# Kernel tuning notes

Hardware: AMD Instinct MI355X
Metric: run time of the kernel (lower is better)

Reference implementation:

```python
import jax, jax.numpy as jnp
import numpy as np

B, H, W, C = 2, 64, 128, 256
HEADS, K, HIDDEN = 8, 9, 1024
HD = C // HEADS
EPS = 1e-5


def _ln(z, g, b):
    m = z.mean(-1, keepdims=True)
    v = ((z - m) ** 2).mean(-1, keepdims=True)
    return (z - m) / jnp.sqrt(v + EPS) * g + b


def _bilinear(img, coords):
    # img: [hd, H, W]; coords: [H, W, K, 2] in [-1, 1] (x=width, y=height), align_corners=True
    Hh, Ww = img.shape[1], img.shape[2]
    cx = (coords[..., 0] + 1.0) * 0.5 * (Ww - 1)
    cy = (coords[..., 1] + 1.0) * 0.5 * (Hh - 1)
    x0 = jnp.floor(cx); y0 = jnp.floor(cy)
    wx = cx - x0; wy = cy - y0
    x0i = jnp.clip(x0, 0, Ww - 1).astype(jnp.int32)
    x1i = jnp.clip(x0 + 1, 0, Ww - 1).astype(jnp.int32)
    y0i = jnp.clip(y0, 0, Hh - 1).astype(jnp.int32)
    y1i = jnp.clip(y0 + 1, 0, Hh - 1).astype(jnp.int32)
    g = lambda yi, xi: img[:, yi, xi]  # [hd, H, W, K]
    return (g(y0i, x0i) * (1 - wy) * (1 - wx) + g(y0i, x1i) * (1 - wy) * wx
            + g(y1i, x0i) * wy * (1 - wx) + g(y1i, x1i) * wy * wx)


def setup_inputs() -> dict:
    key = jax.random.key(0)
    ks = jax.random.split(key, 12)
    s = 0.02
    return {
        "x": jax.random.normal(ks[0], (B, H * W, C), jnp.float32),
        "ref_point": jax.random.uniform(ks[1], (1, H, W, K, 2), jnp.float32, -1.0, 1.0),
        "ln1_g": jnp.ones((C,), jnp.float32), "ln1_b": jnp.zeros((C,), jnp.float32),
        "w_v": jax.random.normal(ks[2], (C, C), jnp.float32) * s, "b_v": jnp.zeros((C,), jnp.float32),
        "w_off": jax.random.normal(ks[3], (C, HEADS * K * 2), jnp.float32) * s, "b_off": jnp.zeros((HEADS * K * 2,), jnp.float32),
        "w_attn": jax.random.normal(ks[4], (C, HEADS * K), jnp.float32) * s, "b_attn": jnp.zeros((HEADS * K,), jnp.float32),
        "w_out": jax.random.normal(ks[5], (C, C), jnp.float32) * s, "b_out": jnp.zeros((C,), jnp.float32),
        "ln2_g": jnp.ones((C,), jnp.float32), "ln2_b": jnp.zeros((C,), jnp.float32),
        "w1": jax.random.normal(ks[6], (C, HIDDEN), jnp.float32) * s, "b1": jnp.zeros((HIDDEN,), jnp.float32),
        "w_dw": jax.random.normal(ks[7], (HIDDEN, 1, 3, 3), jnp.float32) * s, "b_dw": jnp.zeros((HIDDEN,), jnp.float32),
        "w2": jax.random.normal(ks[8], (HIDDEN, C), jnp.float32) * s, "b2": jnp.zeros((C,), jnp.float32),
    }


def reference(x, ref_point, ln1_g, ln1_b, w_v, b_v, w_off, b_off, w_attn, b_attn,
              w_out, b_out, ln2_g, ln2_b, w1, b1, w_dw, b_dw, w2, b2):
    # --- Sphere deformable self-attention branch ---
    xn = _ln(x, ln1_g, ln1_b).reshape(B, H, W, C)
    v = (xn @ w_v + b_v).reshape(B, H, W, HEADS, HD)
    v = jnp.transpose(v, (0, 3, 4, 1, 2))                               # [B, heads, hd, H, W]
    off = (xn @ w_off + b_off).reshape(B, H, W, HEADS, K, 2)
    locs = ref_point[:, :, :, None, :, :] + off                          # [B, H, W, heads, K, 2]
    locs = jnp.transpose(locs, (0, 3, 1, 2, 4, 5))                       # [B, heads, H, W, K, 2]
    attn = jax.nn.softmax((xn @ w_attn + b_attn).reshape(B, H, W, HEADS, K), axis=-1)
    sampled = jax.vmap(jax.vmap(_bilinear))(v, locs)                     # [B, heads, hd, H, W, K]
    agg = jnp.einsum('bndhwk,bhwnk->bhwnd', sampled, attn).reshape(B, H, W, C)
    x = x + ((agg @ w_out) + b_out).reshape(B, H * W, C)
    # --- LeFF branch: linear -> GELU -> circular-pad depthwise conv -> GELU -> linear ---
    y = _ln(x, ln2_g, ln2_b)
    h = jax.nn.gelu(y @ w1 + b1, approximate=False).reshape(B, H, W, HIDDEN)
    h = jnp.transpose(h, (0, 3, 1, 2))                                   # NCHW
    h = jnp.pad(h, ((0, 0), (0, 0), (0, 0), (1, 1)), mode='wrap')        # circular pad along width
    h = jnp.pad(h, ((0, 0), (0, 0), (1, 1), (0, 0)))                     # zero pad along height
    h = jax.lax.conv_general_dilated(h, w_dw, (1, 1), 'VALID',
                                     feature_group_count=HIDDEN,
                                     dimension_numbers=('NCHW', 'OIHW', 'NCHW'))
    h = jax.nn.gelu(h + b_dw[None, :, None, None], approximate=False)
    h = jnp.transpose(h, (0, 2, 3, 1)).reshape(B, H * W, HIDDEN)
    return x + h @ w2 + b2
```

## Files before the change

### kernel.cpp

```cpp
#include <hip/hip_runtime.h>
#include <hip/hip_bf16.h>
#include <hip/hip_fp8.h>
#include <type_traits>

constexpr int Bc = 2, Hc = 64, Wc = 128, Cc = 256;
constexpr int HEADS = 8, KPT = 9, HIDDEN = 1024;
constexpr int HD = Cc / HEADS;
constexpr int NPIX = Hc * Wc;
constexpr int Mrows = Bc * NPIX;
constexpr int NQKV = 512;

typedef __attribute__((ext_vector_type(4))) float f32x4;
typedef __attribute__((ext_vector_type(8))) short bf16x8;

__device__ __forceinline__ float bf2f(unsigned short u) {
    union { unsigned int i; float f; } c; c.i = ((unsigned int)u) << 16; return c.f;
}
__device__ __forceinline__ unsigned short f2bf(float f) {
    __hip_bfloat16 h = __float2bfloat16(f);
    return *reinterpret_cast<unsigned short*>(&h);
}
__device__ __forceinline__ unsigned char f2fp8(float f) {
    return __hip_fp8_e4m3(f).__x;
}
__device__ __forceinline__ float fp82f(unsigned char u) {
    __hip_fp8_e4m3 v; v.__x = u; return (float)v;
}
__device__ __forceinline__ float gelu_exact(float x) {
    return 0.5f * x * (1.0f + erff(x * 0.70710678118654752f));
}
__device__ __forceinline__ void gl2lds16(const void* g, void* l) {
    __builtin_amdgcn_global_load_lds(
        (const __attribute__((address_space(1))) unsigned int*)g,
        (__attribute__((address_space(3))) unsigned int*)l, 16, 0, 0);
}

__global__ __launch_bounds__(256) void prepln_kernel(
        const float* __restrict__ x, const float* __restrict__ ln1_g,
        const float* __restrict__ ln1_b, unsigned short* __restrict__ xn,
        const float* __restrict__ w_v, const float* __restrict__ b_v,
        const float* __restrict__ w_off, const float* __restrict__ b_off,
        const float* __restrict__ w_attn, const float* __restrict__ b_attn,
        const float* __restrict__ w_out, const float* __restrict__ w1,
        const float* __restrict__ w2, const float* __restrict__ w_dw,
        unsigned short* __restrict__ qkvT, float* __restrict__ qkvB,
        unsigned short* __restrict__ woutT, unsigned short* __restrict__ w1T,
        unsigned char* __restrict__ w2T8, float* __restrict__ wdwT) {
    const int t = threadIdx.x;
    if (blockIdx.x < Mrows / 4) {
        const int r = blockIdx.x * 4 + (t >> 6);
        const int l = t & 63;
        const size_t base = (size_t)r * Cc + l * 4;
        const float4 v = *reinterpret_cast<const float4*>(x + base);
        float s  = v.x + v.y + v.z + v.w;
        float s2 = v.x * v.x + v.y * v.y + v.z * v.z + v.w * v.w;
        #pragma unroll
        for (int o = 32; o > 0; o >>= 1) { s += __shfl_down(s, o); s2 += __shfl_down(s2, o); }
        s = __shfl(s, 0); s2 = __shfl(s2, 0);
        const float mean = s * (1.0f / Cc);
        const float rstd = rsqrtf(s2 * (1.0f / Cc) - mean * mean + 1e-5f);
        const float4 gv = *reinterpret_cast<const float4*>(ln1_g + l * 4);
        const float4 bv = *reinterpret_cast<const float4*>(ln1_b + l * 4);
        ushort4 o;
        o.x = f2bf((v.x - mean) * rstd * gv.x + bv.x);
        o.y = f2bf((v.y - mean) * rstd * gv.y + bv.y);
        o.z = f2bf((v.z - mean) * rstd * gv.z + bv.z);
        o.w = f2bf((v.w - mean) * rstd * gv.w + bv.w);
        *reinterpret_cast<ushort4*>(xn + base) = o;
        return;
    }
    const int blk = blockIdx.x - Mrows / 4;
    if (blk < NQKV) {
        const int n = blk;
        float val = 0.0f;
        if (n < 256)       val = w_v[t * 256 + n];
        else if (n < 400)  val = w_off[t * 144 + (n - 256)];
        else if (n < 472)  val = w_attn[t * 72 + (n - 400)];
        qkvT[n * 256 + t] = f2bf(val);
        if (t == 0) {
            float bv = 0.0f;
            if (n < 256)      bv = b_v[n];
            else if (n < 400) bv = b_off[n - 256];
            else if (n < 472) bv = b_attn[n - 400];
            qkvB[n] = bv;
        }
    } else if (blk < NQKV + 256) {
        const int n = blk - NQKV;
        woutT[n * 256 + t] = f2bf(w_out[t * 256 + n]);
    } else if (blk < NQKV + 256 + 1024) {
        const int n = blk - (NQKV + 256);
        w1T[n * 256 + t] = f2bf(w1[t * 1024 + n]);
    } else if (blk < NQKV + 256 + 1024 + 256) {
        const int n = blk - (NQKV + 256 + 1024);
        #pragma unroll
        for (int k = t; k < 1024; k += 256)
            w2T8[n * 1024 + k] = f2fp8(w2[k * 256 + n] * 32.0f);
    } else {
        const int j = blk - (NQKV + 256 + 1024 + 256);
        #pragma unroll
        for (int c = t; c < HIDDEN; c += 256)
            wdwT[j * HIDDEN + c] = w_dw[c * 9 + j];
    }
}

template<int BN, bool GELU, bool RESID, typename TO>
__global__ __launch_bounds__(512) void mfma_gemm(
        const unsigned short* __restrict__ A,
        const unsigned short* __restrict__ BT,
        const float* __restrict__ bias,
        const float* __restrict__ resid,
        TO* __restrict__ Out,
        int N, int K) {
    constexpr int WCOLS = (BN == 128) ? 4 : 2;
    constexpr int WROWS = 8 / WCOLS;
    constexpr int MI = 128 / (WROWS * 16);
    constexpr int NI = BN / (WCOLS * 16);
    constexpr int ACH = 2;
    constexpr int BCH = (BN / 8) / 8;
    constexpr int LA = ACH + BCH;
    constexpr int BUFB = 16384 + BN * 128;
    __shared__ __align__(16) char lds[2 * BUFB];
    const int t = threadIdx.x;
    const int w = t >> 6;
    const int l = t & 63;
    const int row0 = blockIdx.x * 128;
    const int col0 = blockIdx.y * BN;
    const int wr = (w / WCOLS) * (MI * 16);
    const int wc = (w % WCOLS) * (NI * 16);

    const int srow = l >> 3;
    const int selem = ((l & 7) ^ srow) * 8;

    auto stage = [&](char* buf, int k0) {
        unsigned short* As_ = (unsigned short*)buf;
        unsigned short* Bs_ = (unsigned short*)(buf + 16384);
        #pragma unroll
        for (int i = 0; i < ACH; ++i) {
            const int c = w + i * 8;
            const int row = c * 8 + srow;
            gl2lds16(A + (size_t)(row0 + row) * K + k0 + selem, As_ + c * 512);
        }
        #pragma unroll
        for (int i = 0; i < BCH; ++i) {
            const int c = w + i * 8;
            const int row = c * 8 + srow;
            gl2lds16(BT + (size_t)(col0 + row) * K + k0 + selem, Bs_ + c * 512);
        }
    };

    f32x4 acc[MI][NI] = {};
    const int nt = K / 64;

    stage(lds, 0);
    stage(lds + BUFB, 64);

    for (int tt = 0; tt < nt; ++tt) {
        if (tt + 1 < nt) {
            if constexpr (LA == 4) asm volatile("s_waitcnt vmcnt(4)" ::: "memory");
            else                   asm volatile("s_waitcnt vmcnt(3)" ::: "memory");
        } else {
            asm volatile("s_waitcnt vmcnt(0)" ::: "memory");
        }
        __builtin_amdgcn_s_barrier();
        __builtin_amdgcn_sched_barrier(0);

        const char* Ab = lds + (size_t)(tt & 1) * BUFB;
        const char* Bb = Ab + 16384;
        #pragma unroll
        for (int ks = 0; ks < 2; ++ks) {
            const int kb = ks * 64 + (l >> 4) * 16;
            bf16x8 af[MI], bfr[NI];
            #pragma unroll
            for (int mi = 0; mi < MI; ++mi) {
                const int row = wr + mi * 16 + (l & 15);
                af[mi] = *(const bf16x8*)(Ab + row * 128 + (kb ^ ((row & 7) << 4)));
            }
            #pragma unroll
            for (int ni = 0; ni < NI; ++ni) {
                const int row = wc + ni * 16 + (l & 15);
                bfr[ni] = *(const bf16x8*)(Bb + row * 128 + (kb ^ ((row & 7) << 4)));
            }
            #pragma unroll
            for (int mi = 0; mi < MI; ++mi)
                #pragma unroll
                for (int ni = 0; ni < NI; ++ni)
                    acc[mi][ni] = __builtin_amdgcn_mfma_f32_16x16x32_bf16(
                        af[mi], bfr[ni], acc[mi][ni], 0, 0, 0);
        }
        __builtin_amdgcn_s_barrier();
        __builtin_amdgcn_sched_barrier(0);
        if (tt + 2 < nt) stage(lds + (size_t)(tt & 1) * BUFB, (tt + 2) * 64);
    }

    constexpr int ROWB = BN * (int)sizeof(TO);
    const int lrow = (l >> 4) * 4;
    const int lcol = l & 15;
    #pragma unroll
    for (int ni = 0; ni < NI; ++ni) {
        const int col = wc + ni * 16 + lcol;
        const float bb = bias[col0 + col];
        #pragma unroll
        for (int mi = 0; mi < MI; ++mi) {
            #pragma unroll
            for (int r = 0; r < 4; ++r) {
                const int row = wr + mi * 16 + lrow + r;
                float v = acc[mi][ni][r] + bb;
                if constexpr (GELU) v = gelu_exact(v);
                if constexpr (std::is_same<TO, unsigned short>::value) {
                    *(unsigned short*)(lds + row * ROWB + ((col * 2) ^ ((row & 7) << 4))) = f2bf(v);
                } else if constexpr (std::is_same<TO, unsigned char>::value) {
                    *(unsigned char*)(lds + row * ROWB + ((col) ^ ((row & 7) << 4))) = f2fp8(v);
                } else {
                    *(float*)(lds + row * ROWB + ((col * 4) ^ ((row & 7) << 4))) = v;
                }
            }
        }
    }
    __syncthreads();
    constexpr int CPR = ROWB / 16;
    constexpr int RPI = 512 / CPR;
    const int ck = t % CPR;
    #pragma unroll
    for (int it = 0; it < 128 / RPI; ++it) {
        const int row = (t / CPR) + it * RPI;
        const int bo = ck * 16;
        const char* src = lds + row * ROWB + (bo ^ ((row & 7) << 4));
        if constexpr (std::is_same<TO, unsigned short>::value) {
            *(int4*)(Out + (size_t)(row0 + row) * N + col0 + bo / 2) = *(const int4*)src;
        } else if constexpr (std::is_same<TO, unsigned char>::value) {
            *(int4*)(Out + (size_t)(row0 + row) * N + col0 + bo) = *(const int4*)src;
        } else {
            float4 val = *(const float4*)src;
            if constexpr (RESID) {
                const float4 rv = *(const float4*)(resid + (size_t)(row0 + row) * N + col0 + bo / 4);
                val.x += rv.x; val.y += rv.y; val.z += rv.z; val.w += rv.w;
            }
            *(float4*)((float*)Out + (size_t)(row0 + row) * N + col0 + bo / 4) = val;
        }
    }
}

__global__ __launch_bounds__(512) void qkv_gemm(
        const unsigned short* __restrict__ A,
        const unsigned short* __restrict__ BT,
        const float* __restrict__ bias,
        unsigned char* __restrict__ Fv,
        unsigned short* __restrict__ Foa,
        int K) {
    constexpr int BN = 128;
    constexpr int MI = 4, NI = 2;
    constexpr int BUFB = 16384 + BN * 128;
    __shared__ __align__(16) char lds[2 * BUFB];
    const int t = threadIdx.x;
    const int w = t >> 6;
    const int l = t & 63;
    const int row0 = blockIdx.x * 128;
    const int col0 = blockIdx.y * BN;
    const int wr = (w / 4) * 64;
    const int wc = (w % 4) * 32;

    const int srow = l >> 3;
    const int selem = ((l & 7) ^ srow) * 8;

    auto stage = [&](char* buf, int k0) {
        unsigned short* As_ = (unsigned short*)buf;
        unsigned short* Bs_ = (unsigned short*)(buf + 16384);
        #pragma unroll
        for (int i = 0; i < 2; ++i) {
            const int c = w + i * 8;
            const int row = c * 8 + srow;
            gl2lds16(A + (size_t)(row0 + row) * K + k0 + selem, As_ + c * 512);
        }
        #pragma unroll
        for (int i = 0; i < 2; ++i) {
            const int c = w + i * 8;
            const int row = c * 8 + srow;
            gl2lds16(BT + (size_t)(col0 + row) * K + k0 + selem, Bs_ + c * 512);
        }
    };

    f32x4 acc[MI][NI] = {};
    stage(lds, 0);
    stage(lds + BUFB, 64);

    for (int tt = 0; tt < 4; ++tt) {
        if (tt + 1 < 4) asm volatile("s_waitcnt vmcnt(4)" ::: "memory");
        else            asm volatile("s_waitcnt vmcnt(0)" ::: "memory");
        __builtin_amdgcn_s_barrier();
        __builtin_amdgcn_sched_barrier(0);

        const char* Ab = lds + (size_t)(tt & 1) * BUFB;
        const char* Bb = Ab + 16384;
        #pragma unroll
        for (int ks = 0; ks < 2; ++ks) {
            const int kb = ks * 64 + (l >> 4) * 16;
            bf16x8 af[MI], bfr[NI];
            #pragma unroll
            for (int mi = 0; mi < MI; ++mi) {
                const int row = wr + mi * 16 + (l & 15);
                af[mi] = *(const bf16x8*)(Ab + row * 128 + (kb ^ ((row & 7) << 4)));
            }
            #pragma unroll
            for (int ni = 0; ni < NI; ++ni) {
                const int row = wc + ni * 16 + (l & 15);
                bfr[ni] = *(const bf16x8*)(Bb + row * 128 + (kb ^ ((row & 7) << 4)));
            }
            #pragma unroll
            for (int mi = 0; mi < MI; ++mi)
                #pragma unroll
                for (int ni = 0; ni < NI; ++ni)
                    acc[mi][ni] = __builtin_amdgcn_mfma_f32_16x16x32_bf16(
                        af[mi], bfr[ni], acc[mi][ni], 0, 0, 0);
        }
        __builtin_amdgcn_s_barrier();
        __builtin_amdgcn_sched_barrier(0);
        if (tt + 2 < 4) stage(lds + (size_t)(tt & 1) * BUFB, (tt + 2) * 64);
    }

    const int lrow = (l >> 4) * 4;
    const int lcol = l & 15;
    if (col0 < 256) {
        #pragma unroll
        for (int ni = 0; ni < NI; ++ni) {
            const int col = wc + ni * 16 + lcol;
            const float bb = bias[col0 + col];
            #pragma unroll
            for (int mi = 0; mi < MI; ++mi) {
                #pragma unroll
                for (int r = 0; r < 4; ++r) {
                    const int row = wr + mi * 16 + lrow + r;
                    *(unsigned char*)(lds + row * 128 + (col ^ ((row & 7) << 4)))
                        = f2fp8(acc[mi][ni][r] + bb);
                }
            }
        }
        __syncthreads();
        const int ck = t & 7;
        #pragma unroll
        for (int it = 0; it < 2; ++it) {
            const int row = (t >> 3) + it * 64;
            const int bo = ck * 16;
            *(int4*)(Fv + (size_t)(row0 + row) * 256 + col0 + bo)
                = *(const int4*)(lds + row * 128 + (bo ^ ((row & 7) << 4)));
        }
    } else {
        #pragma unroll
        for (int ni = 0; ni < NI; ++ni) {
            const int col = wc + ni * 16 + lcol;
            const float bb = bias[col0 + col];
            #pragma unroll
            for (int mi = 0; mi < MI; ++mi) {
                #pragma unroll
                for (int r = 0; r < 4; ++r) {
                    const int row = wr + mi * 16 + lrow + r;
                    *(unsigned short*)(lds + row * 256 + ((col * 2) ^ ((row & 7) << 4)))
                        = f2bf(acc[mi][ni][r] + bb);
                }
            }
        }
        __syncthreads();
        const int ck = t & 15;
        #pragma unroll
        for (int it = 0; it < 4; ++it) {
            const int row = (t >> 4) + it * 32;
            const int bo = ck * 16;
            *(int4*)(Foa + (size_t)(row0 + row) * 256 + (col0 - 256) + bo / 2)
                = *(const int4*)(lds + row * 256 + (bo ^ ((row & 7) << 4)));
        }
    }
}

__global__ __launch_bounds__(512) void w2_gemm_fp8(
        const unsigned char* __restrict__ A,
        const unsigned char* __restrict__ BT,
        const float* __restrict__ bias,
        const unsigned short* __restrict__ x2b,
        float* __restrict__ Out,
        int N, int K) {
    constexpr int ABYTES = 128 * 128;
    constexpr int BUFB = ABYTES + 64 * 128;
    __shared__ __align__(16) char lds[2 * BUFB];
    const int t = threadIdx.x;
    const int w = t >> 6;
    const int l = t & 63;
    const int row0 = blockIdx.x * 128;
    const int col0 = blockIdx.y * 64;
    const int wr = (w >> 1) * 32;
    const int wc = (w & 1) * 32;

    const int srow = l >> 3;
    const int sbyte = ((l & 7) ^ srow) * 16;

    auto stage = [&](char* buf, int k0) {
        unsigned char* As_ = (unsigned char*)buf;
        unsigned char* Bs_ = (unsigned char*)(buf + ABYTES);
        #pragma unroll
        for (int i = 0; i < 2; ++i) {
            const int c = w + i * 8;
            const int row = c * 8 + srow;
            gl2lds16(A + (size_t)(row0 + row) * K + k0 + sbyte, As_ + c * 1024);
        }
        {
            const int row = w * 8 + srow;
            gl2lds16(BT + (size_t)(col0 + row) * K + k0 + sbyte, Bs_ + w * 1024);
        }
    };

    f32x4 acc[2][2] = {};
    const int nt = K / 128;

    stage(lds, 0);
    stage(lds + BUFB, 128);

    for (int tt = 0; tt < nt; ++tt) {
        if (tt + 1 < nt) asm volatile("s_waitcnt vmcnt(3)" ::: "memory");
        else             asm volatile("s_waitcnt vmcnt(0)" ::: "memory");
        __builtin_amdgcn_s_barrier();
        __builtin_amdgcn_sched_barrier(0);

        const char* Ab = lds + (size_t)(tt & 1) * BUFB;
        const char* Bb = Ab + ABYTES;
        #pragma unroll
        for (int ks = 0; ks < 4; ++ks) {
            const int kb = ks * 32 + (l >> 4) * 8;
            long af[2], bfr[2];
            #pragma unroll
            for (int mi = 0; mi < 2; ++mi) {
                const int row = wr + mi * 16 + (l & 15);
                af[mi] = *(const long*)(Ab + row * 128 + (kb ^ ((row & 7) << 4)));
            }
            #pragma unroll
            for (int ni = 0; ni < 2; ++ni) {
                const int row = wc + ni * 16 + (l & 15);
                bfr[ni] = *(const long*)(Bb + row * 128 + (kb ^ ((row & 7) << 4)));
            }
            #pragma unroll
            for (int mi = 0; mi < 2; ++mi)
                #pragma unroll
                for (int ni = 0; ni < 2; ++ni)
                    acc[mi][ni] = __builtin_amdgcn_mfma_f32_16x16x32_fp8_fp8(
                        af[mi], bfr[ni], acc[mi][ni], 0, 0, 0);
        }
        __builtin_amdgcn_s_barrier();
        __builtin_amdgcn_sched_barrier(0);
        if (tt + 2 < nt) stage(lds + (size_t)(tt & 1) * BUFB, (tt + 2) * 128);
    }

    const int lrow = (l >> 4) * 4;
    const int lcol = l & 15;
    #pragma unroll
    for (int ni = 0; ni < 2; ++ni) {
        const int col = wc + ni * 16 + lcol;
        const float bb = bias[col0 + col];
        #pragma unroll
        for (int mi = 0; mi < 2; ++mi) {
            #pragma unroll
            for (int r = 0; r < 4; ++r) {
                const int row = wr + mi * 16 + lrow + r;
                *(float*)(lds + row * 256 + ((col * 4) ^ ((row & 7) << 4)))
                    = acc[mi][ni][r] * 0.03125f + bb;
            }
        }
    }
    __syncthreads();
    const int ck = t & 15;
    #pragma unroll
    for (int it = 0; it < 4; ++it) {
        const int row = (t >> 4) + it * 32;
        const int bo = ck * 16;
        float4 val = *(const float4*)(lds + row * 256 + (bo ^ ((row & 7) << 4)));
        const ushort4 rv = *(const ushort4*)(x2b + (size_t)(row0 + row) * N + col0 + bo / 4);
        val.x += bf2f(rv.x); val.y += bf2f(rv.y); val.z += bf2f(rv.z); val.w += bf2f(rv.w);
        *(float4*)(Out + (size_t)(row0 + row) * N + col0 + bo / 4) = val;
    }
}

__global__ __launch_bounds__(512) void wout_ln2_kernel(
        const unsigned short* __restrict__ A,
        const unsigned short* __restrict__ BT,
        const float* __restrict__ bias,
        const float* __restrict__ resid,
        const float* __restrict__ g2, const float* __restrict__ b2,
        unsigned short* __restrict__ X2,
        unsigned short* __restrict__ Y) {
    constexpr int BM = 32, K = 256;
    constexpr int ABYTES = BM * 128;
    constexpr int BUFB = ABYTES + 256 * 128;
    __shared__ __align__(16) char lds[2 * BUFB];
    const int t = threadIdx.x;
    const int w = t >> 6;
    const int l = t & 63;
    const int row0 = blockIdx.x * BM;
    const int wr = (w >> 2) * 16;
    const int wc = (w & 3) * 64;

    const int srow = l >> 3;
    const int selem = ((l & 7) ^ srow) * 8;

    auto stage = [&](char* buf, int k0) {
        unsigned short* As_ = (unsigned short*)buf;
        unsigned short* Bs_ = (unsigned short*)(buf + ABYTES);
        if (w < 4) {
            const int row = w * 8 + srow;
            gl2lds16(A + (size_t)(row0 + row) * K + k0 + selem, As_ + w * 512);
        }
        #pragma unroll
        for (int i = 0; i < 4; ++i) {
            const int c = w + i * 8;
            const int row = c * 8 + srow;
            gl2lds16(BT + (size_t)row * K + k0 + selem, Bs_ + c * 512);
        }
    };

    f32x4 acc[1][4] = {};
    stage(lds, 0);
    stage(lds + BUFB, 64);

    for (int tt = 0; tt < 4; ++tt) {
        if (tt + 1 < 4) {
            if (w < 4) asm volatile("s_waitcnt vmcnt(5)" ::: "memory");
            else       asm volatile("s_waitcnt vmcnt(4)" ::: "memory");
        } else {
            asm volatile("s_waitcnt vmcnt(0)" ::: "memory");
        }
        __builtin_amdgcn_s_barrier();
        __builtin_amdgcn_sched_barrier(0);

        const char* Ab = lds + (size_t)(tt & 1) * BUFB;
        const char* Bb = Ab + ABYTES;
        #pragma unroll
        for (int ks = 0; ks < 2; ++ks) {
            const int kb = ks * 64 + (l >> 4) * 16;
            bf16x8 af, bfr[4];
            {
                const int row = wr + (l & 15);
                af = *(const bf16x8*)(Ab + row * 128 + (kb ^ ((row & 7) << 4)));
            }
            #pragma unroll
            for (int ni = 0; ni < 4; ++ni) {
                const int row = wc + ni * 16 + (l & 15);
                bfr[ni] = *(const bf16x8*)(Bb + row * 128 + (kb ^ ((row & 7) << 4)));
            }
            #pragma unroll
            for (int ni = 0; ni < 4; ++ni)
                acc[0][ni] = __builtin_amdgcn_mfma_f32_16x16x32_bf16(
                    af, bfr[ni], acc[0][ni], 0, 0, 0);
        }
        __builtin_amdgcn_s_barrier();
        __builtin_amdgcn_sched_barrier(0);
        if (tt + 2 < 4) stage(lds + (size_t)(tt & 1) * BUFB, (tt + 2) * 64);
    }

    const int lrow = (l >> 4) * 4;
    const int lcol = l & 15;
    #pragma unroll
    for (int ni = 0; ni < 4; ++ni) {
        const int col = wc + ni * 16 + lcol;
        const float bb = bias[col];
        #pragma unroll
        for (int r = 0; r < 4; ++r) {
            const int row = wr + lrow + r;
            *(float*)(lds + row * 1024 + ((col * 4) ^ ((row & 7) << 4))) = acc[0][ni][r] + bb;
        }
    }
    __syncthreads();
    const float4 gv = *reinterpret_cast<const float4*>(g2 + l * 4);
    const float4 bv = *reinterpret_cast<const float4*>(b2 + l * 4);
    #pragma unroll
    for (int it = 0; it < 4; ++it) {
        const int r = w + it * 8;
        float4 v = *(const float4*)(lds + r * 1024 + ((l * 16) ^ ((r & 7) << 4)));
        const float4 rv = *(const float4*)(resid + (size_t)(row0 + r) * Cc + l * 4);
        v.x += rv.x; v.y += rv.y; v.z += rv.z; v.w += rv.w;
        float s  = v.x + v.y + v.z + v.w;
        float s2 = v.x * v.x + v.y * v.y + v.z * v.z + v.w * v.w;
        #pragma unroll
        for (int o = 32; o > 0; o >>= 1) { s += __shfl_down(s, o); s2 += __shfl_down(s2, o); }
        s = __shfl(s, 0); s2 = __shfl(s2, 0);
        const float mean = s * (1.0f / Cc);
        const float rstd = rsqrtf(s2 * (1.0f / Cc) - mean * mean + 1e-5f);
        ushort4 xo;
        xo.x = f2bf(v.x); xo.y = f2bf(v.y); xo.z = f2bf(v.z); xo.w = f2bf(v.w);
        *(ushort4*)(X2 + (size_t)(row0 + r) * Cc + l * 4) = xo;
        ushort4 o;
        o.x = f2bf((v.x - mean) * rstd * gv.x + bv.x);
        o.y = f2bf((v.y - mean) * rstd * gv.y + bv.y);
        o.z = f2bf((v.z - mean) * rstd * gv.z + bv.z);
        o.w = f2bf((v.w - mean) * rstd * gv.w + bv.w);
        *(ushort4*)(Y + (size_t)(row0 + r) * Cc + l * 4) = o;
    }
}

__global__ __launch_bounds__(256) void sample_kernel(const unsigned char* __restrict__ Fv,
        const unsigned short* __restrict__ Foa,
        const float* __restrict__ refp, unsigned short* __restrict__ agg) {
    constexpr int PPB = 4;
    constexpr int nblk = Mrows / PPB;
    const int bid = blockIdx.x;
    const int qi = (bid & 7) * (nblk / 8) + (bid >> 3);
    const int m0 = qi * PPB;
    const int b = m0 / NPIX;
    const int pix0 = m0 - b * NPIX;
    const int t = threadIdx.x;
    __shared__ int4   s_idx[PPB][72];
    __shared__ float4 s_w[PPB][72];
    __shared__ float  s_lg[PPB][72];

    for (int idx = t; idx < PPB * 72; idx += 256) {
        const int p = idx / 72, hk = idx - p * 72;
        const int head = hk / 9, k = hk - head * 9;
        const int m = m0 + p, pix = pix0 + p;
        const size_t fb = (size_t)m * 256;
        const unsigned int ou = *(const unsigned int*)(Foa + fb + head * 18 + k * 2);
        const float ox = __uint_as_float(ou << 16);
        const float oy = __uint_as_float(ou & 0xffff0000u);
        const float2 rr = *(const float2*)(refp + ((size_t)pix * KPT + k) * 2);
        const float cx = (rr.x + ox + 1.0f) * 0.5f * (Wc - 1);
        const float cy = (rr.y + oy + 1.0f) * 0.5f * (Hc - 1);
        const float fx = floorf(cx), fy = floorf(cy);
        const float wx = cx - fx, wy = cy - fy;
        const int x0 = min(max((int)fx, 0), Wc - 1);
        const int x1 = min(max((int)fx + 1, 0), Wc - 1);
        const int y0 = min(max((int)fy, 0), Hc - 1);
        const int y1 = min(max((int)fy + 1, 0), Hc - 1);
        s_idx[p][hk] = make_int4(y0 * Wc + x0, y0 * Wc + x1, y1 * Wc + x0, y1 * Wc + x1);
        s_w[p][hk] = make_float4((1.0f - wy) * (1.0f - wx), (1.0f - wy) * wx,
                                 wy * (1.0f - wx), wy * wx);
        s_lg[p][hk] = bf2f(Foa[fb + 144 + hk]);
    }
    __syncthreads();
    for (int idx = t; idx < PPB * 72; idx += 256) {
        const int p = idx / 72, hk = idx - p * 72;
        const int h9 = (hk / 9) * 9;
        float mx = -1e30f;
        #pragma unroll
        for (int k = 0; k < 9; ++k) mx = fmaxf(mx, s_lg[p][h9 + k]);
        float sm = 0.0f;
        #pragma unroll
        for (int k = 0; k < 9; ++k) sm += __expf(s_lg[p][h9 + k] - mx);
        const float a = __expf(s_lg[p][hk] - mx) / sm;
        float4 w = s_w[p][hk];
        w.x *= a; w.y *= a; w.z *= a; w.w *= a;
        s_w[p][hk] = w;
    }
    __syncthreads();
    const int p = t >> 6, tl = t & 63;
    const int head = tl >> 3, dq = tl & 7;
    const unsigned char* vb = Fv + (size_t)b * NPIX * 256 + head * HD + dq * 4;
    float a0 = 0.f, a1 = 0.f, a2 = 0.f, a3 = 0.f;
    #pragma unroll
    for (int k = 0; k < 9; ++k) {
        const int hk = head * 9 + k;
        const int4   ix = s_idx[p][hk];
        const float4 ww = s_w[p][hk];
        {
            const uchar4 u = *(const uchar4*)(vb + (size_t)ix.x * 256);
            a0 += fp82f(u.x) * ww.x; a1 += fp82f(u.y) * ww.x;
            a2 += fp82f(u.z) * ww.x; a3 += fp82f(u.w) * ww.x;
        }
        {
            const uchar4 u = *(const uchar4*)(vb + (size_t)ix.y * 256);
            a0 += fp82f(u.x) * ww.y; a1 += fp82f(u.y) * ww.y;
            a2 += fp82f(u.z) * ww.y; a3 += fp82f(u.w) * ww.y;
        }
        {
            const uchar4 u = *(const uchar4*)(vb + (size_t)ix.z * 256);
            a0 += fp82f(u.x) * ww.z; a1 += fp82f(u.y) * ww.z;
            a2 += fp82f(u.z) * ww.z; a3 += fp82f(u.w) * ww.z;
        }
        {
            const uchar4 u = *(const uchar4*)(vb + (size_t)ix.w * 256);
            a0 += fp82f(u.x) * ww.w; a1 += fp82f(u.y) * ww.w;
            a2 += fp82f(u.z) * ww.w; a3 += fp82f(u.w) * ww.w;
        }
    }
    ushort4 o;
    o.x = f2bf(a0); o.y = f2bf(a1); o.z = f2bf(a2); o.w = f2bf(a3);
    *reinterpret_cast<ushort4*>(agg + (size_t)(m0 + p) * Cc + tl * 4) = o;
}

__global__ __launch_bounds__(256) void dwconv_kernel(const unsigned char* __restrict__ h,
        const float* __restrict__ wdwT, const float* __restrict__ bdw,
        unsigned char* __restrict__ h2) {
    constexpr int NQ = 8;
    constexpr int nblk = Mrows / NQ;
    const int bid = blockIdx.x;
    const int qi = (bid & 7) * (nblk / 8) + (bid >> 3);
    const int m0 = qi * NQ;
    const int b = m0 / NPIX;
    const int pix0 = m0 - b * NPIX;
    const int y = pix0 / Wc, x0 = pix0 - y * Wc;
    const int t = threadIdx.x;
    const int c0 = t * 4;

    float wreg[9][4];
    #pragma unroll
    for (int j = 0; j < 9; ++j) {
        const float4 wv = *reinterpret_cast<const float4*>(wdwT + j * HIDDEN + c0);
        wreg[j][0] = wv.x; wreg[j][1] = wv.y; wreg[j][2] = wv.z; wreg[j][3] = wv.w;
    }

    float acc[NQ][4] = {};
    #pragma unroll
    for (int dy = -1; dy <= 1; ++dy) {
        const int yy = y + dy;
        if (yy < 0 || yy >= Hc) continue;
        const size_t rowbase = ((size_t)b * NPIX + (size_t)yy * Wc) * HIDDEN + c0;
        #pragma unroll
        for (int j = 0; j < NQ + 2; ++j) {
            const int xx = (x0 + j - 1 + Wc) & (Wc - 1);
            const uchar4 hv = *reinterpret_cast<const uchar4*>(h + rowbase + (size_t)xx * HIDDEN);
            const float f0 = fp82f(hv.x), f1 = fp82f(hv.y), f2 = fp82f(hv.z), f3 = fp82f(hv.w);
            #pragma unroll
            for (int q = 0; q < NQ; ++q) {
                if (q >= j - 2 && q <= j) {
                    const int wj = (dy + 1) * 3 + (j - q);
                    acc[q][0] += f0 * wreg[wj][0];
                    acc[q][1] += f1 * wreg[wj][1];
                    acc[q][2] += f2 * wreg[wj][2];
                    acc[q][3] += f3 * wreg[wj][3];
                }
            }
        }
    }
    const float4 bb = *reinterpret_cast<const float4*>(bdw + c0);
    #pragma unroll
    for (int q = 0; q < NQ; ++q) {
        uchar4 o;
        o.x = f2fp8(gelu_exact(acc[q][0] + bb.x));
        o.y = f2fp8(gelu_exact(acc[q][1] + bb.y));
        o.z = f2fp8(gelu_exact(acc[q][2] + bb.z));
        o.w = f2fp8(gelu_exact(acc[q][3] + bb.w));
        *reinterpret_cast<uchar4*>(h2 + (size_t)(m0 + q) * HIDDEN + c0) = o;
    }
}

extern "C" void kernel_launch(void* const* d_in, const int* in_sizes, int n_in,
                              void* d_out, int out_size, void* d_ws, size_t ws_size,
                              hipStream_t stream) {
    const float* x      = (const float*)d_in[0];
    const float* refp   = (const float*)d_in[1];
    const float* ln1_g  = (const float*)d_in[2];
    const float* ln1_b  = (const float*)d_in[3];
    const float* w_v    = (const float*)d_in[4];
    const float* b_v    = (const float*)d_in[5];
    const float* w_off  = (const float*)d_in[6];
    const float* b_off  = (const float*)d_in[7];
    const float* w_attn = (const float*)d_in[8];
    const float* b_attn = (const float*)d_in[9];
    const float* w_out  = (const float*)d_in[10];
    const float* b_out  = (const float*)d_in[11];
    const float* ln2_g  = (const float*)d_in[12];
    const float* ln2_b  = (const float*)d_in[13];
    const float* w1     = (const float*)d_in[14];
    const float* b1     = (const float*)d_in[15];
    const float* w_dw   = (const float*)d_in[16];
    const float* b_dw   = (const float*)d_in[17];
    const float* w2     = (const float*)d_in[18];
    const float* b2     = (const float*)d_in[19];
    float* out = (float*)d_out;

    char* wsb = (char*)d_ws;
    unsigned short* Abuf = (unsigned short*)(wsb);
    unsigned short* Foa  = (unsigned short*)(wsb + (8ull  << 20));
    unsigned char*  Fv   = (unsigned char*)(wsb + (16ull << 20));
    unsigned short* ybuf = (unsigned short*)(wsb + (8ull  << 20));
    unsigned short* x2b  = (unsigned short*)(wsb + (16ull << 20));
    unsigned char*  hbuf = (unsigned char*)(wsb + (32ull << 20));
    unsigned char*  h2   = (unsigned char*)(wsb + (48ull << 20));
    size_t woff = 64ull << 20;
    unsigned short* qkvT = (unsigned short*)(wsb + woff); woff += (size_t)NQKV * 256 * 2;
    unsigned short* woutT= (unsigned short*)(wsb + woff); woff += 256 * 256 * 2;
    unsigned short* w1T  = (unsigned short*)(wsb + woff); woff += 1024 * 256 * 2;
    unsigned char*  w2T8 = (unsigned char*)(wsb + woff);  woff += 256 * 1024;
    float*          wdwT = (float*)(wsb + woff);          woff += 9 * 1024 * 4;
    float*          qkvB = (float*)(wsb + woff);

    prepln_kernel<<<Mrows / 4 + NQKV + 256 + 1024 + 256 + 9, 256, 0, stream>>>(
        x, ln1_g, ln1_b, Abuf,
        w_v, b_v, w_off, b_off, w_attn, b_attn, w_out, w1, w2, w_dw,
        qkvT, qkvB, woutT, w1T, w2T8, wdwT);
    qkv_gemm<<<dim3(Mrows / 128, NQKV / 128), 512, 0, stream>>>(
        Abuf, qkvT, qkvB, Fv, Foa, 256);
    sample_kernel<<<Mrows / 4, 256, 0, stream>>>(Fv, Foa, refp, Abuf);
    wout_ln2_kernel<<<Mrows / 32, 512, 0, stream>>>(
        Abuf, woutT, b_out, x, ln2_g, ln2_b, x2b, ybuf);
    mfma_gemm<128, true, false, unsigned char><<<dim3(Mrows / 128, 1024 / 128), 512, 0, stream>>>(
        ybuf, w1T, b1, nullptr, hbuf, 1024, 256);
    dwconv_kernel<<<Mrows / 8, 256, 0, stream>>>(hbuf, wdwT, b_dw, h2);
    w2_gemm_fp8<<<dim3(Mrows / 128, 256 / 64), 512, 0, stream>>>(
        h2, w2T8, b2, x2b, out, 256, 1024);
}
```

Measured before the change: 111.1 us.

## Run W1 GEMM in FP8 and switch GELU to fast tanh-style approximation

The first LeFF linear layer now takes FP8 activations (the LN2 output is written as FP8) and FP8 pre-scaled w1 weights, and runs through a generalized fp8_gemm template in place of the bf16 MFMA GEMM. The bf16 GEMM template is removed. Exact erf GELU is replaced everywhere by a sigmoid-form tanh approximation using __expf. This halves operand bytes and uses the faster FP8 MFMA path, and lowers GELU cost, at the price of extra precision loss in the LN2 output and in the activations.

```diff
diff --git a/kernel.cpp b/kernel.cpp
--- a/kernel.cpp
+++ b/kernel.cpp
@@ -26,8 +26,8 @@
 __device__ __forceinline__ float fp82f(unsigned char u) {
     __hip_fp8_e4m3 v; v.__x = u; return (float)v;
 }
-__device__ __forceinline__ float gelu_exact(float x) {
-    return 0.5f * x * (1.0f + erff(x * 0.70710678118654752f));
+__device__ __forceinline__ float gelu_fast(float x) {
+    return x / (1.0f + __expf(-1.5957691216f * (x + 0.044715f * x * x * x)));
 }
 __device__ __forceinline__ void gl2lds16(const void* g, void* l) {
     __builtin_amdgcn_global_load_lds(
@@ -44,7 +44,7 @@
         const float* __restrict__ w_out, const float* __restrict__ w1,
         const float* __restrict__ w2, const float* __restrict__ w_dw,
         unsigned short* __restrict__ qkvT, float* __restrict__ qkvB,
-        unsigned short* __restrict__ woutT, unsigned short* __restrict__ w1T,
+        unsigned short* __restrict__ woutT, unsigned char* __restrict__ w1T8,
         unsigned char* __restrict__ w2T8, float* __restrict__ wdwT) {
     const int t = threadIdx.x;
     if (blockIdx.x < Mrows / 4) {
@@ -89,7 +89,7 @@
         woutT[n * 256 + t] = f2bf(w_out[t * 256 + n]);
     } else if (blk < NQKV + 256 + 1024) {
         const int n = blk - (NQKV + 256);
-        w1T[n * 256 + t] = f2bf(w1[t * 1024 + n]);
+        w1T8[n * 256 + t] = f2fp8(w1[t * 1024 + n] * 32.0f);
     } else if (blk < NQKV + 256 + 1024 + 256) {
         const int n = blk - (NQKV + 256 + 1024);
         #pragma unroll
@@ -100,143 +100,6 @@
         #pragma unroll
         for (int c = t; c < HIDDEN; c += 256)
             wdwT[j * HIDDEN + c] = w_dw[c * 9 + j];
-    }
-}
-
-template<int BN, bool GELU, bool RESID, typename TO>
-__global__ __launch_bounds__(512) void mfma_gemm(
-        const unsigned short* __restrict__ A,
-        const unsigned short* __restrict__ BT,
-        const float* __restrict__ bias,
-        const float* __restrict__ resid,
-        TO* __restrict__ Out,
-        int N, int K) {
-    constexpr int WCOLS = (BN == 128) ? 4 : 2;
-    constexpr int WROWS = 8 / WCOLS;
-    constexpr int MI = 128 / (WROWS * 16);
-    constexpr int NI = BN / (WCOLS * 16);
-    constexpr int ACH = 2;
-    constexpr int BCH = (BN / 8) / 8;
-    constexpr int LA = ACH + BCH;
-    constexpr int BUFB = 16384 + BN * 128;
-    __shared__ __align__(16) char lds[2 * BUFB];
-    const int t = threadIdx.x;
-    const int w = t >> 6;
-    const int l = t & 63;
-    const int row0 = blockIdx.x * 128;
-    const int col0 = blockIdx.y * BN;
-    const int wr = (w / WCOLS) * (MI * 16);
-    const int wc = (w % WCOLS) * (NI * 16);
-
-    const int srow = l >> 3;
-    const int selem = ((l & 7) ^ srow) * 8;
-
-    auto stage = [&](char* buf, int k0) {
-        unsigned short* As_ = (unsigned short*)buf;
-        unsigned short* Bs_ = (unsigned short*)(buf + 16384);
-        #pragma unroll
-        for (int i = 0; i < ACH; ++i) {
-            const int c = w + i * 8;
-            const int row = c * 8 + srow;
-            gl2lds16(A + (size_t)(row0 + row) * K + k0 + selem, As_ + c * 512);
-        }
-        #pragma unroll
-        for (int i = 0; i < BCH; ++i) {
-            const int c = w + i * 8;
-            const int row = c * 8 + srow;
-            gl2lds16(BT + (size_t)(col0 + row) * K + k0 + selem, Bs_ + c * 512);
-        }
-    };
-
-    f32x4 acc[MI][NI] = {};
-    const int nt = K / 64;
-
-    stage(lds, 0);
-    stage(lds + BUFB, 64);
-
-    for (int tt = 0; tt < nt; ++tt) {
-        if (tt + 1 < nt) {
-            if constexpr (LA == 4) asm volatile("s_waitcnt vmcnt(4)" ::: "memory");
-            else                   asm volatile("s_waitcnt vmcnt(3)" ::: "memory");
-        } else {
-            asm volatile("s_waitcnt vmcnt(0)" ::: "memory");
-        }
-        __builtin_amdgcn_s_barrier();
-        __builtin_amdgcn_sched_barrier(0);
-
-        const char* Ab = lds + (size_t)(tt & 1) * BUFB;
-        const char* Bb = Ab + 16384;
-        #pragma unroll
-        for (int ks = 0; ks < 2; ++ks) {
-            const int kb = ks * 64 + (l >> 4) * 16;
-            bf16x8 af[MI], bfr[NI];
-            #pragma unroll
-            for (int mi = 0; mi < MI; ++mi) {
-                const int row = wr + mi * 16 + (l & 15);
-                af[mi] = *(const bf16x8*)(Ab + row * 128 + (kb ^ ((row & 7) << 4)));
-            }
-            #pragma unroll
-            for (int ni = 0; ni < NI; ++ni) {
-                const int row = wc + ni * 16 + (l & 15);
-                bfr[ni] = *(const bf16x8*)(Bb + row * 128 + (kb ^ ((row & 7) << 4)));
-            }
-            #pragma unroll
-            for (int mi = 0; mi < MI; ++mi)
-                #pragma unroll
-                for (int ni = 0; ni < NI; ++ni)
-                    acc[mi][ni] = __builtin_amdgcn_mfma_f32_16x16x32_bf16(
-                        af[mi], bfr[ni], acc[mi][ni], 0, 0, 0);
-        }
-        __builtin_amdgcn_s_barrier();
-        __builtin_amdgcn_sched_barrier(0);
-        if (tt + 2 < nt) stage(lds + (size_t)(tt & 1) * BUFB, (tt + 2) * 64);
-    }
-
-    constexpr int ROWB = BN * (int)sizeof(TO);
-    const int lrow = (l >> 4) * 4;
-    const int lcol = l & 15;
-    #pragma unroll
-    for (int ni = 0; ni < NI; ++ni) {
-        const int col = wc + ni * 16 + lcol;
-        const float bb = bias[col0 + col];
-        #pragma unroll
-        for (int mi = 0; mi < MI; ++mi) {
-            #pragma unroll
-            for (int r = 0; r < 4; ++r) {
-                const int row = wr + mi * 16 + lrow + r;
-                float v = acc[mi][ni][r] + bb;
-                if constexpr (GELU) v = gelu_exact(v);
-                if constexpr (std::is_same<TO, unsigned short>::value) {
-                    *(unsigned short*)(lds + row * ROWB + ((col * 2) ^ ((row & 7) << 4))) = f2bf(v);
-                } else if constexpr (std::is_same<TO, unsigned char>::value) {
-                    *(unsigned char*)(lds + row * ROWB + ((col) ^ ((row & 7) << 4))) = f2fp8(v);
-                } else {
-                    *(float*)(lds + row * ROWB + ((col * 4) ^ ((row & 7) << 4))) = v;
-                }
-            }
-        }
-    }
-    __syncthreads();
-    constexpr int CPR = ROWB / 16;
-    constexpr int RPI = 512 / CPR;
-    const int ck = t % CPR;
-    #pragma unroll
-    for (int it = 0; it < 128 / RPI; ++it) {
-        const int row = (t / CPR) + it * RPI;
-        const int bo = ck * 16;
-        const char* src = lds + row * ROWB + (bo ^ ((row & 7) << 4));
-        if constexpr (std::is_same<TO, unsigned short>::value) {
-            *(int4*)(Out + (size_t)(row0 + row) * N + col0 + bo / 2) = *(const int4*)src;
-        } else if constexpr (std::is_same<TO, unsigned char>::value) {
-            *(int4*)(Out + (size_t)(row0 + row) * N + col0 + bo) = *(const int4*)src;
-        } else {
-            float4 val = *(const float4*)src;
-            if constexpr (RESID) {
-                const float4 rv = *(const float4*)(resid + (size_t)(row0 + row) * N + col0 + bo / 4);
-                val.x += rv.x; val.y += rv.y; val.z += rv.z; val.w += rv.w;
-            }
-            *(float4*)((float*)Out + (size_t)(row0 + row) * N + col0 + bo / 4) = val;
-        }
     }
 }
 
@@ -370,12 +233,13 @@
     }
 }
 
-__global__ __launch_bounds__(512) void w2_gemm_fp8(
+template<bool GELU, bool RESID, typename TO>
+__global__ __launch_bounds__(512) void fp8_gemm(
         const unsigned char* __restrict__ A,
         const unsigned char* __restrict__ BT,
         const float* __restrict__ bias,
-        const unsigned short* __restrict__ x2b,
-        float* __restrict__ Out,
+        const unsigned short* __restrict__ residb,
+        TO* __restrict__ Out,
         int N, int K) {
     constexpr int ABYTES = 128 * 128;
     constexpr int BUFB = ABYTES + 64 * 128;
@@ -446,6 +310,7 @@
         if (tt + 2 < nt) stage(lds + (size_t)(tt & 1) * BUFB, (tt + 2) * 128);
     }
 
+    constexpr int ROWB = 64 * (int)sizeof(TO);
     const int lrow = (l >> 4) * 4;
     const int lcol = l & 15;
     #pragma unroll
@@ -457,21 +322,38 @@
             #pragma unroll
             for (int r = 0; r < 4; ++r) {
                 const int row = wr + mi * 16 + lrow + r;
-                *(float*)(lds + row * 256 + ((col * 4) ^ ((row & 7) << 4)))
-                    = acc[mi][ni][r] * 0.03125f + bb;
+                const int xm = ((row & 7) << 4) & (ROWB - 1);
+                float v = acc[mi][ni][r] * 0.03125f + bb;
+                if constexpr (GELU) v = gelu_fast(v);
+                if constexpr (std::is_same<TO, unsigned char>::value) {
+                    *(unsigned char*)(lds + row * ROWB + (col ^ xm)) = f2fp8(v);
+                } else {
+                    *(float*)(lds + row * ROWB + ((col * 4) ^ xm)) = v;
+                }
             }
         }
     }
     __syncthreads();
-    const int ck = t & 15;
-    #pragma unroll
-    for (int it = 0; it < 4; ++it) {
-        const int row = (t >> 4) + it * 32;
+    constexpr int CPR = ROWB / 16;
+    constexpr int RPI = 512 / CPR;
+    const int ck = t % CPR;
+    #pragma unroll
+    for (int it = 0; it < 128 / RPI; ++it) {
+        const int row = (t / CPR) + it * RPI;
         const int bo = ck * 16;
-        float4 val = *(const float4*)(lds + row * 256 + (bo ^ ((row & 7) << 4)));
-        const ushort4 rv = *(const ushort4*)(x2b + (size_t)(row0 + row) * N + col0 + bo / 4);
-        val.x += bf2f(rv.x); val.y += bf2f(rv.y); val.z += bf2f(rv.z); val.w += bf2f(rv.w);
-        *(float4*)(Out + (size_t)(row0 + row) * N + col0 + bo / 4) = val;
+        const int xm = ((row & 7) << 4) & (ROWB - 1);
+        const char* src = lds + row * ROWB + (bo ^ xm);
+        if constexpr (std::is_same<TO, unsigned char>::value) {
+            *(int4*)(Out + (size_t)(row0 + row) * N + col0 + bo) = *(const int4*)src;
+        } else {
+            float4 val = *(const float4*)src;
+            if constexpr (RESID) {
+                const ushort4 rv = *(const ushort4*)(residb + (size_t)(row0 + row) * N + col0 + bo / 4);
+                val.x += bf2f(rv.x); val.y += bf2f(rv.y);
+                val.z += bf2f(rv.z); val.w += bf2f(rv.w);
+            }
+            *(float4*)((float*)Out + (size_t)(row0 + row) * N + col0 + bo / 4) = val;
+        }
     }
 }
 
@@ -482,7 +364,7 @@
         const float* __restrict__ resid,
         const float* __restrict__ g2, const float* __restrict__ b2,
         unsigned short* __restrict__ X2,
-        unsigned short* __restrict__ Y) {
+        unsigned char* __restrict__ Y) {
     constexpr int BM = 32, K = 256;
     constexpr int ABYTES = BM * 128;
     constexpr int BUFB = ABYTES + 256 * 128;
@@ -582,12 +464,12 @@
         ushort4 xo;
         xo.x = f2bf(v.x); xo.y = f2bf(v.y); xo.z = f2bf(v.z); xo.w = f2bf(v.w);
         *(ushort4*)(X2 + (size_t)(row0 + r) * Cc + l * 4) = xo;
-        ushort4 o;
-        o.x = f2bf((v.x - mean) * rstd * gv.x + bv.x);
-        o.y = f2bf((v.y - mean) * rstd * gv.y + bv.y);
-        o.z = f2bf((v.z - mean) * rstd * gv.z + bv.z);
-        o.w = f2bf((v.w - mean) * rstd * gv.w + bv.w);
-        *(ushort4*)(Y + (size_t)(row0 + r) * Cc + l * 4) = o;
+        uchar4 o;
+        o.x = f2fp8((v.x - mean) * rstd * gv.x + bv.x);
+        o.y = f2fp8((v.y - mean) * rstd * gv.y + bv.y);
+        o.z = f2fp8((v.z - mean) * rstd * gv.z + bv.z);
+        o.w = f2fp8((v.w - mean) * rstd * gv.w + bv.w);
+        *(uchar4*)(Y + (size_t)(row0 + r) * Cc + l * 4) = o;
     }
 }
 
@@ -727,10 +609,10 @@
     #pragma unroll
     for (int q = 0; q < NQ; ++q) {
         uchar4 o;
-        o.x = f2fp8(gelu_exact(acc[q][0] + bb.x));
-        o.y = f2fp8(gelu_exact(acc[q][1] + bb.y));
-        o.z = f2fp8(gelu_exact(acc[q][2] + bb.z));
-        o.w = f2fp8(gelu_exact(acc[q][3] + bb.w));
+        o.x = f2fp8(gelu_fast(acc[q][0] + bb.x));
+        o.y = f2fp8(gelu_fast(acc[q][1] + bb.y));
+        o.z = f2fp8(gelu_fast(acc[q][2] + bb.z));
+        o.w = f2fp8(gelu_fast(acc[q][3] + bb.w));
         *reinterpret_cast<uchar4*>(h2 + (size_t)(m0 + q) * HIDDEN + c0) = o;
     }
 }
@@ -764,14 +646,14 @@
     unsigned short* Abuf = (unsigned short*)(wsb);
     unsigned short* Foa  = (unsigned short*)(wsb + (8ull  << 20));
     unsigned char*  Fv   = (unsigned char*)(wsb + (16ull << 20));
-    unsigned short* ybuf = (unsigned short*)(wsb + (8ull  << 20));
+    unsigned char*  ybuf8= (unsigned char*)(wsb + (8ull  << 20));
     unsigned short* x2b  = (unsigned short*)(wsb + (16ull << 20));
     unsigned char*  hbuf = (unsigned char*)(wsb + (32ull << 20));
     unsigned char*  h2   = (unsigned char*)(wsb + (48ull << 20));
     size_t woff = 64ull << 20;
     unsigned short* qkvT = (unsigned short*)(wsb + woff); woff += (size_t)NQKV * 256 * 2;
     unsigned short* woutT= (unsigned short*)(wsb + woff); woff += 256 * 256 * 2;
-    unsigned short* w1T  = (unsigned short*)(wsb + woff); woff += 1024 * 256 * 2;
+    unsigned char*  w1T8 = (unsigned char*)(wsb + woff);  woff += 1024 * 256;
     unsigned char*  w2T8 = (unsigned char*)(wsb + woff);  woff += 256 * 1024;
     float*          wdwT = (float*)(wsb + woff);          woff += 9 * 1024 * 4;
     float*          qkvB = (float*)(wsb + woff);
@@ -779,15 +661,15 @@
     prepln_kernel<<<Mrows / 4 + NQKV + 256 + 1024 + 256 + 9, 256, 0, stream>>>(
         x, ln1_g, ln1_b, Abuf,
         w_v, b_v, w_off, b_off, w_attn, b_attn, w_out, w1, w2, w_dw,
-        qkvT, qkvB, woutT, w1T, w2T8, wdwT);
+        qkvT, qkvB, woutT, w1T8, w2T8, wdwT);
     qkv_gemm<<<dim3(Mrows / 128, NQKV / 128), 512, 0, stream>>>(
         Abuf, qkvT, qkvB, Fv, Foa, 256);
     sample_kernel<<<Mrows / 4, 256, 0, stream>>>(Fv, Foa, refp, Abuf);
     wout_ln2_kernel<<<Mrows / 32, 512, 0, stream>>>(
-        Abuf, woutT, b_out, x, ln2_g, ln2_b, x2b, ybuf);
-    mfma_gemm<128, true, false, unsigned char><<<dim3(Mrows / 128, 1024 / 128), 512, 0, stream>>>(
-        ybuf, w1T, b1, nullptr, hbuf, 1024, 256);
+        Abuf, woutT, b_out, x, ln2_g, ln2_b, x2b, ybuf8);
+    fp8_gemm<true, false, unsigned char><<<dim3(Mrows / 128, 1024 / 64), 512, 0, stream>>>(
+        ybuf8, w1T8, b1, nullptr, hbuf, 1024, 256);
     dwconv_kernel<<<Mrows / 8, 256, 0, stream>>>(hbuf, wdwT, b_dw, h2);
-    w2_gemm_fp8<<<dim3(Mrows / 128, 256 / 64), 512, 0, stream>>>(
+    fp8_gemm<false, true, float><<<dim3(Mrows / 128, 256 / 64), 512, 0, stream>>>(
         h2, w2T8, b2, x2b, out, 256, 1024);
 }
```

New measurement: 113.0 us. Within noise of the previous version (+1.7%).
